# Kernel tuning notes

Hardware: AMD Instinct MI355X
Metric: run time of the kernel (lower is better)

The kernel has to match this reference:

```python
import jax, jax.numpy as jnp
import numpy as np

NUM_REGIONS = 32  # region ids 1..32; id 0 is background, excluded like torch.unique()[ids>0]


def setup_inputs() -> dict:
    key = jax.random.key(0)
    k1, k2 = jax.random.split(key)
    B, T, C, D, H, W = 2, 8, 64, 48, 48, 48
    features = jax.random.normal(k1, (B, T, C, D, H, W), dtype=jnp.float32)
    segmentation = jax.random.randint(k2, (B, 1, D, H, W), 0, NUM_REGIONS + 1, dtype=jnp.int32)
    return {"features": features, "segmentation": segmentation}


def reference(features, segmentation):
    # features: [B, T, C, D, H, W], segmentation: [B, 1, D, H, W] (int region ids)
    B, T, C, D, H, W = features.shape
    N = D * H * W
    seg = segmentation.reshape(B, N)                 # [B, N]
    feats = features.reshape(B, T, C, N)             # [B, T, C, N]

    def per_batch(f, s):
        # f: [T, C, N], s: [N]
        fv = f.reshape(T * C, N).T                   # [N, T*C] voxel-major
        sums = jax.ops.segment_sum(fv, s, num_segments=NUM_REGIONS + 1)          # [R+1, T*C]
        counts = jax.ops.segment_sum(jnp.ones((N,), f.dtype), s,
                                     num_segments=NUM_REGIONS + 1)               # [R+1]
        # mean per region; empty regions stay zero (torch code `continue`s, leaving zeros)
        means = jnp.where(counts[:, None] > 0,
                          sums / jnp.maximum(counts, 1.0)[:, None],
                          0.0)
        return means[1:].reshape(NUM_REGIONS, T, C).transpose(1, 0, 2)           # [T, R, C]

    return jax.vmap(per_batch)(feats, seg)          # [B, T, num_regions, feature_dim]
```

## Files before the change

kernel.cpp:

```cpp
#include <hip/hip_runtime.h>
#include <hip/hip_bf16.h>


#define BB 2
#define TT 8
#define CC 64
#define NVOX 110592
#define NREG 32
#define RS 33
#define VW 256
#define BLKV 1024
#define NBBT 108
#define PART_OFF 2048
#define MST 68
#define MCP 2176

typedef __attribute__((ext_vector_type(8))) short bf16x8;
typedef __attribute__((ext_vector_type(4))) float f32x4;

static __device__ __forceinline__ unsigned cvtpk(float x, float y) {
    __hip_bfloat162 h = __float22bfloat162_rn(make_float2(x, y));
    unsigned u;
    __builtin_memcpy(&u, &h, 4);
    return u;
}
static __device__ __forceinline__ float lowf(unsigned w)  { return __builtin_bit_cast(float, w << 16); }
static __device__ __forceinline__ float highf(unsigned w) { return __builtin_bit_cast(float, w & 0xFFFF0000u); }

struct HiLo { uint4 h, l; };
static __device__ __forceinline__ HiLo split8(const f32x4& a, const f32x4& b) {
    HiLo r;
    r.h.x = cvtpk(a[0], a[1]); r.h.y = cvtpk(a[2], a[3]);
    r.h.z = cvtpk(b[0], b[1]); r.h.w = cvtpk(b[2], b[3]);
    r.l.x = cvtpk(a[0] - lowf(r.h.x), a[1] - highf(r.h.x));
    r.l.y = cvtpk(a[2] - lowf(r.h.y), a[3] - highf(r.h.y));
    r.l.z = cvtpk(b[0] - lowf(r.h.z), b[1] - highf(r.h.z));
    r.l.w = cvtpk(b[2] - lowf(r.h.w), b[3] - highf(r.h.w));
    return r;
}
static __device__ __forceinline__ bf16x8 asbf(const uint4& u) {
    bf16x8 v;
    __builtin_memcpy(&v, &u, 16);
    return v;
}
static __device__ __forceinline__ bf16x8 bfrag(const int4& s0, const int4& s1, int r) {
    uint4 u;
    u.x = (s0.x == r ? 0x3F80u : 0u) | (s0.y == r ? 0x3F800000u : 0u);
    u.y = (s0.z == r ? 0x3F80u : 0u) | (s0.w == r ? 0x3F800000u : 0u);
    u.z = (s1.x == r ? 0x3F80u : 0u) | (s1.y == r ? 0x3F800000u : 0u);
    u.w = (s1.z == r ? 0x3F80u : 0u) | (s1.w == r ? 0x3F800000u : 0u);
    return asbf(u);
}

struct Ld {
    f32x4 q0a, q0b, q1a, q1b, q2a, q2b, q3a, q3b;
    int4 s0, s1;
};
static __device__ __forceinline__ void ldtile(Ld& L, const float* fp0, const float* fp1,
                                              const float* fp2, const float* fp3,
                                              const int* sp, int kv) {
    L.q0a = *(const f32x4*)(fp0 + kv); L.q0b = *(const f32x4*)(fp0 + kv + 4);
    L.q1a = *(const f32x4*)(fp1 + kv); L.q1b = *(const f32x4*)(fp1 + kv + 4);
    L.q2a = *(const f32x4*)(fp2 + kv); L.q2b = *(const f32x4*)(fp2 + kv + 4);
    L.q3a = *(const f32x4*)(fp3 + kv); L.q3b = *(const f32x4*)(fp3 + kv + 4);
    L.s0 = *(const int4*)(sp + kv);    L.s1 = *(const int4*)(sp + kv + 4);
}
#define MFMA __builtin_amdgcn_mfma_f32_16x16x32_bf16
static __device__ __forceinline__ void proc(const Ld& L, int r0, int r1,
        f32x4& a00, f32x4& a01, f32x4& a10, f32x4& a11,
        f32x4& a20, f32x4& a21, f32x4& a30, f32x4& a31) {
    const bf16x8 b0 = bfrag(L.s0, L.s1, r0);
    const bf16x8 b1 = bfrag(L.s0, L.s1, r1);
    const HiLo h0 = split8(L.q0a, L.q0b);
    const HiLo h1 = split8(L.q1a, L.q1b);
    const HiLo h2 = split8(L.q2a, L.q2b);
    const HiLo h3 = split8(L.q3a, L.q3b);
    a00 = MFMA(asbf(h0.h), b0, a00, 0, 0, 0);
    a00 = MFMA(asbf(h0.l), b0, a00, 0, 0, 0);
    a01 = MFMA(asbf(h0.h), b1, a01, 0, 0, 0);
    a01 = MFMA(asbf(h0.l), b1, a01, 0, 0, 0);
    a10 = MFMA(asbf(h1.h), b0, a10, 0, 0, 0);
    a10 = MFMA(asbf(h1.l), b0, a10, 0, 0, 0);
    a11 = MFMA(asbf(h1.h), b1, a11, 0, 0, 0);
    a11 = MFMA(asbf(h1.l), b1, a11, 0, 0, 0);
    a20 = MFMA(asbf(h2.h), b0, a20, 0, 0, 0);
    a20 = MFMA(asbf(h2.l), b0, a20, 0, 0, 0);
    a21 = MFMA(asbf(h2.h), b1, a21, 0, 0, 0);
    a21 = MFMA(asbf(h2.l), b1, a21, 0, 0, 0);
    a30 = MFMA(asbf(h3.h), b0, a30, 0, 0, 0);
    a30 = MFMA(asbf(h3.l), b0, a30, 0, 0, 0);
    a31 = MFMA(asbf(h3.h), b1, a31, 0, 0, 0);
    a31 = MFMA(asbf(h3.l), b1, a31, 0, 0, 0);
}

__global__ __launch_bounds__(256) void seg_hist(const int* __restrict__ seg,
                                                float* __restrict__ counts) {
    __shared__ float h[4 * RS];
    const int tid = threadIdx.x;
    const int w = tid >> 6;
    for (int i = tid; i < 4 * RS; i += 256) h[i] = 0.f;
    __syncthreads();

    const int base = blockIdx.x * 1024 + tid * 4;
    const int b = base / NVOX;
    const int4 s4 = *(const int4*)(seg + base);
    atomicAdd(&h[w * RS + s4.x], 1.f);
    atomicAdd(&h[w * RS + s4.y], 1.f);
    atomicAdd(&h[w * RS + s4.z], 1.f);
    atomicAdd(&h[w * RS + s4.w], 1.f);
    __syncthreads();

    if (tid < RS) {
        const float v = h[tid] + h[RS + tid] + h[2 * RS + tid] + h[3 * RS + tid];
        atomicAdd(&counts[b * RS + tid], v);
    }
}

__global__ __launch_bounds__(256) void seg_sum(const float* __restrict__ feat,
                                               const int* __restrict__ seg,
                                               float* __restrict__ part) {
    __shared__ float sm[4 * MCP];
    const int tid = threadIdx.x;
    const int w = tid >> 6;
    const int l = tid & 63;
    const int lm = l & 15;
    const int kg = (l >> 4) * 8;
    const int b = blockIdx.z;
    const int t = blockIdx.y;

    const int vw = blockIdx.x * BLKV + w * VW;
    const float* __restrict__ fp0 = feat + (size_t)(b * TT + t) * CC * NVOX
                                    + (size_t)lm * NVOX + vw + kg;
    const float* __restrict__ fp1 = fp0 + (size_t)16 * NVOX;
    const float* __restrict__ fp2 = fp0 + (size_t)32 * NVOX;
    const float* __restrict__ fp3 = fp0 + (size_t)48 * NVOX;
    const int* __restrict__ sp = seg + (size_t)b * NVOX + vw + kg;
    const int r0 = lm + 1;
    const int r1 = lm + 17;

    f32x4 a00 = {0.f, 0.f, 0.f, 0.f}, a01 = a00, a10 = a00, a11 = a00;
    f32x4 a20 = a00, a21 = a00, a30 = a00, a31 = a00;

    Ld A, B;
    ldtile(A, fp0, fp1, fp2, fp3, sp, 0);
    #pragma unroll 1
    for (int j = 0; j < 3; ++j) {
        ldtile(B, fp0, fp1, fp2, fp3, sp, j * 64 + 32);
        proc(A, r0, r1, a00, a01, a10, a11, a20, a21, a30, a31);
        ldtile(A, fp0, fp1, fp2, fp3, sp, j * 64 + 64);
        proc(B, r0, r1, a00, a01, a10, a11, a20, a21, a30, a31);
    }
    ldtile(B, fp0, fp1, fp2, fp3, sp, 224);
    proc(A, r0, r1, a00, a01, a10, a11, a20, a21, a30, a31);
    proc(B, r0, r1, a00, a01, a10, a11, a20, a21, a30, a31);

    float* __restrict__ mt = sm + w * MCP;
    const int rw = (l >> 4) * 4;
    *(f32x4*)(mt + lm * MST + rw)             = a00;
    *(f32x4*)(mt + (lm + 16) * MST + rw)      = a01;
    *(f32x4*)(mt + lm * MST + rw + 16)        = a10;
    *(f32x4*)(mt + (lm + 16) * MST + rw + 16) = a11;
    *(f32x4*)(mt + lm * MST + rw + 32)        = a20;
    *(f32x4*)(mt + (lm + 16) * MST + rw + 32) = a21;
    *(f32x4*)(mt + lm * MST + rw + 48)        = a30;
    *(f32x4*)(mt + (lm + 16) * MST + rw + 48) = a31;
    __syncthreads();

    float* __restrict__ p = part + ((size_t)(b * TT + t) * NBBT + blockIdx.x) * 2048;
    #pragma unroll
    for (int h = 0; h < 2; ++h) {
        const int e = tid * 4 + h * 1024;
        const int idx = (e >> 6) * MST + (e & 63);
        const f32x4 v0 = *(const f32x4*)(sm + idx);
        const f32x4 v1 = *(const f32x4*)(sm + MCP + idx);
        const f32x4 v2 = *(const f32x4*)(sm + 2 * MCP + idx);
        const f32x4 v3 = *(const f32x4*)(sm + 3 * MCP + idx);
        *(f32x4*)(p + e) = (v0 + v1) + (v2 + v3);
    }
}

__global__ __launch_bounds__(64) void seg_div(const float* __restrict__ part,
                                              const float* __restrict__ counts,
                                              float* __restrict__ out) {
    const int i = blockIdx.x * 64 + threadIdx.x;
    const int bt = i >> 11;
    const int b = i >> 14;
    const int r = ((i >> 6) & 31) + 1;
    const float* __restrict__ p = part + (size_t)bt * NBBT * 2048 + (i & 2047);
    float s0 = 0.f, s1 = 0.f, s2 = 0.f, s3 = 0.f;
    #pragma unroll 4
    for (int j = 0; j < NBBT; j += 4) {
        s0 += p[j * 2048];       s1 += p[(j + 1) * 2048];
        s2 += p[(j + 2) * 2048]; s3 += p[(j + 3) * 2048];
    }
    const float cnt = counts[b * RS + r];
    out[i] = cnt > 0.f ? ((s0 + s1) + (s2 + s3)) / cnt : 0.f;
}

extern "C" void kernel_launch(void* const* d_in, const int* in_sizes, int n_in,
                              void* d_out, int out_size, void* d_ws, size_t ws_size,
                              hipStream_t stream) {
    const float* feat = (const float*)d_in[0];
    const int* seg = (const int*)d_in[1];
    float* out = (float*)d_out;
    float* counts = (float*)d_ws;
    float* part = (float*)d_ws + PART_OFF;

    (void)hipMemsetAsync(d_ws, 0, (size_t)(BB * RS) * sizeof(float), stream);

    seg_hist<<<dim3((BB * NVOX) / 1024), 256, 0, stream>>>(seg, counts);
    seg_sum<<<dim3(NVOX / BLKV, TT, BB), 256, 0, stream>>>(feat, seg, part);
    seg_div<<<dim3(out_size / 64), 64, 0, stream>>>(part, counts, out);
}
```

Measured before the change: 610.6 us.

## Split seg_sum waves over channel halves and triple-buffer fully unrolled loads

Each wave now covers 32 channels over 512 voxels instead of 64 channels over 256 voxels, with pairs of waves sharing voxel ranges. This halves the accumulator and load registers per wave, and the launch bound asks for 4 blocks per CU. The voxel loop is fully unrolled with three rotating load buffers, so loads are issued two tiles ahead of the MFMA work. Shared-memory reduction now sums two partial tiles instead of four. The aims are higher occupancy and better latency hiding, at the cost of each wave pair re-reading the same segmentation data.

```diff
diff --git a/kernel.cpp b/kernel.cpp
--- a/kernel.cpp
+++ b/kernel.cpp
@@ -8,12 +8,10 @@
 #define NVOX 110592
 #define NREG 32
 #define RS 33
-#define VW 256
 #define BLKV 1024
 #define NBBT 108
 #define PART_OFF 2048
 #define MST 68
-#define MCP 2176
 
 typedef __attribute__((ext_vector_type(8))) short bf16x8;
 typedef __attribute__((ext_vector_type(4))) float f32x4;
@@ -52,29 +50,21 @@
     return asbf(u);
 }
 
-struct Ld {
-    f32x4 q0a, q0b, q1a, q1b, q2a, q2b, q3a, q3b;
-    int4 s0, s1;
-};
-static __device__ __forceinline__ void ldtile(Ld& L, const float* fp0, const float* fp1,
-                                              const float* fp2, const float* fp3,
-                                              const int* sp, int kv) {
+struct Ld2 { f32x4 q0a, q0b, q1a, q1b; int4 s0, s1; };
+#define MFMA __builtin_amdgcn_mfma_f32_16x16x32_bf16
+
+static __device__ __forceinline__ void ldt(Ld2& L, const float* fp0, const float* fp1,
+                                           const int* sp, int kv) {
     L.q0a = *(const f32x4*)(fp0 + kv); L.q0b = *(const f32x4*)(fp0 + kv + 4);
     L.q1a = *(const f32x4*)(fp1 + kv); L.q1b = *(const f32x4*)(fp1 + kv + 4);
-    L.q2a = *(const f32x4*)(fp2 + kv); L.q2b = *(const f32x4*)(fp2 + kv + 4);
-    L.q3a = *(const f32x4*)(fp3 + kv); L.q3b = *(const f32x4*)(fp3 + kv + 4);
     L.s0 = *(const int4*)(sp + kv);    L.s1 = *(const int4*)(sp + kv + 4);
 }
-#define MFMA __builtin_amdgcn_mfma_f32_16x16x32_bf16
-static __device__ __forceinline__ void proc(const Ld& L, int r0, int r1,
-        f32x4& a00, f32x4& a01, f32x4& a10, f32x4& a11,
-        f32x4& a20, f32x4& a21, f32x4& a30, f32x4& a31) {
+static __device__ __forceinline__ void proc2(const Ld2& L, int r0, int r1,
+        f32x4& a00, f32x4& a01, f32x4& a10, f32x4& a11) {
     const bf16x8 b0 = bfrag(L.s0, L.s1, r0);
     const bf16x8 b1 = bfrag(L.s0, L.s1, r1);
     const HiLo h0 = split8(L.q0a, L.q0b);
     const HiLo h1 = split8(L.q1a, L.q1b);
-    const HiLo h2 = split8(L.q2a, L.q2b);
-    const HiLo h3 = split8(L.q3a, L.q3b);
     a00 = MFMA(asbf(h0.h), b0, a00, 0, 0, 0);
     a00 = MFMA(asbf(h0.l), b0, a00, 0, 0, 0);
     a01 = MFMA(asbf(h0.h), b1, a01, 0, 0, 0);
@@ -83,14 +73,6 @@
     a10 = MFMA(asbf(h1.l), b0, a10, 0, 0, 0);
     a11 = MFMA(asbf(h1.h), b1, a11, 0, 0, 0);
     a11 = MFMA(asbf(h1.l), b1, a11, 0, 0, 0);
-    a20 = MFMA(asbf(h2.h), b0, a20, 0, 0, 0);
-    a20 = MFMA(asbf(h2.l), b0, a20, 0, 0, 0);
-    a21 = MFMA(asbf(h2.h), b1, a21, 0, 0, 0);
-    a21 = MFMA(asbf(h2.l), b1, a21, 0, 0, 0);
-    a30 = MFMA(asbf(h3.h), b0, a30, 0, 0, 0);
-    a30 = MFMA(asbf(h3.l), b0, a30, 0, 0, 0);
-    a31 = MFMA(asbf(h3.h), b1, a31, 0, 0, 0);
-    a31 = MFMA(asbf(h3.l), b1, a31, 0, 0, 0);
 }
 
 __global__ __launch_bounds__(256) void seg_hist(const int* __restrict__ seg,
@@ -116,66 +98,69 @@
     }
 }
 
-__global__ __launch_bounds__(256) void seg_sum(const float* __restrict__ feat,
-                                               const int* __restrict__ seg,
-                                               float* __restrict__ part) {
-    __shared__ float sm[4 * MCP];
+__global__ __launch_bounds__(256, 4) void seg_sum(const float* __restrict__ feat,
+                                                  const int* __restrict__ seg,
+                                                  float* __restrict__ part) {
+    __shared__ float sm[2 * NREG * MST];
     const int tid = threadIdx.x;
     const int w = tid >> 6;
     const int l = tid & 63;
     const int lm = l & 15;
     const int kg = (l >> 4) * 8;
+    const int h = w & 1;
+    const int v = w >> 1;
     const int b = blockIdx.z;
     const int t = blockIdx.y;
 
-    const int vw = blockIdx.x * BLKV + w * VW;
+    const int vw = blockIdx.x * BLKV + v * 512;
     const float* __restrict__ fp0 = feat + (size_t)(b * TT + t) * CC * NVOX
-                                    + (size_t)lm * NVOX + vw + kg;
+                                    + (size_t)(32 * h + lm) * NVOX + vw + kg;
     const float* __restrict__ fp1 = fp0 + (size_t)16 * NVOX;
-    const float* __restrict__ fp2 = fp0 + (size_t)32 * NVOX;
-    const float* __restrict__ fp3 = fp0 + (size_t)48 * NVOX;
     const int* __restrict__ sp = seg + (size_t)b * NVOX + vw + kg;
     const int r0 = lm + 1;
     const int r1 = lm + 17;
 
     f32x4 a00 = {0.f, 0.f, 0.f, 0.f}, a01 = a00, a10 = a00, a11 = a00;
-    f32x4 a20 = a00, a21 = a00, a30 = a00, a31 = a00;
 
-    Ld A, B;
-    ldtile(A, fp0, fp1, fp2, fp3, sp, 0);
-    #pragma unroll 1
-    for (int j = 0; j < 3; ++j) {
-        ldtile(B, fp0, fp1, fp2, fp3, sp, j * 64 + 32);
-        proc(A, r0, r1, a00, a01, a10, a11, a20, a21, a30, a31);
-        ldtile(A, fp0, fp1, fp2, fp3, sp, j * 64 + 64);
-        proc(B, r0, r1, a00, a01, a10, a11, a20, a21, a30, a31);
-    }
-    ldtile(B, fp0, fp1, fp2, fp3, sp, 224);
-    proc(A, r0, r1, a00, a01, a10, a11, a20, a21, a30, a31);
-    proc(B, r0, r1, a00, a01, a10, a11, a20, a21, a30, a31);
+    Ld2 S0, S1, S2;
+    #define LDJ(S, J)  ldt(S, fp0, fp1, sp, (J) * 32)
+    #define PRC(S)     proc2(S, r0, r1, a00, a01, a10, a11)
+    LDJ(S0, 0); LDJ(S1, 1);
+    PRC(S0); LDJ(S2, 2);
+    PRC(S1); LDJ(S0, 3);
+    PRC(S2); LDJ(S1, 4);
+    PRC(S0); LDJ(S2, 5);
+    PRC(S1); LDJ(S0, 6);
+    PRC(S2); LDJ(S1, 7);
+    PRC(S0); LDJ(S2, 8);
+    PRC(S1); LDJ(S0, 9);
+    PRC(S2); LDJ(S1, 10);
+    PRC(S0); LDJ(S2, 11);
+    PRC(S1); LDJ(S0, 12);
+    PRC(S2); LDJ(S1, 13);
+    PRC(S0); LDJ(S2, 14);
+    PRC(S1); LDJ(S0, 15);
+    PRC(S2);
+    PRC(S0);
+    #undef LDJ
+    #undef PRC
 
-    float* __restrict__ mt = sm + w * MCP;
-    const int rw = (l >> 4) * 4;
-    *(f32x4*)(mt + lm * MST + rw)             = a00;
-    *(f32x4*)(mt + (lm + 16) * MST + rw)      = a01;
-    *(f32x4*)(mt + lm * MST + rw + 16)        = a10;
-    *(f32x4*)(mt + (lm + 16) * MST + rw + 16) = a11;
-    *(f32x4*)(mt + lm * MST + rw + 32)        = a20;
-    *(f32x4*)(mt + (lm + 16) * MST + rw + 32) = a21;
-    *(f32x4*)(mt + lm * MST + rw + 48)        = a30;
-    *(f32x4*)(mt + (lm + 16) * MST + rw + 48) = a31;
+    float* __restrict__ mt = sm + v * (NREG * MST);
+    const int cb = 32 * h + (l >> 4) * 4;
+    *(f32x4*)(mt + lm * MST + cb)             = a00;
+    *(f32x4*)(mt + (lm + 16) * MST + cb)      = a01;
+    *(f32x4*)(mt + lm * MST + cb + 16)        = a10;
+    *(f32x4*)(mt + (lm + 16) * MST + cb + 16) = a11;
     __syncthreads();
 
     float* __restrict__ p = part + ((size_t)(b * TT + t) * NBBT + blockIdx.x) * 2048;
     #pragma unroll
-    for (int h = 0; h < 2; ++h) {
-        const int e = tid * 4 + h * 1024;
+    for (int g = 0; g < 2; ++g) {
+        const int e = tid * 4 + g * 1024;
         const int idx = (e >> 6) * MST + (e & 63);
         const f32x4 v0 = *(const f32x4*)(sm + idx);
-        const f32x4 v1 = *(const f32x4*)(sm + MCP + idx);
-        const f32x4 v2 = *(const f32x4*)(sm + 2 * MCP + idx);
-        const f32x4 v3 = *(const f32x4*)(sm + 3 * MCP + idx);
-        *(f32x4*)(p + e) = (v0 + v1) + (v2 + v3);
+        const f32x4 v1 = *(const f32x4*)(sm + NREG * MST + idx);
+        *(f32x4*)(p + e) = v0 + v1;
     }
 }
 
```

New measurement: 610.1 us. No clear change (-0.1%).
